# Kernel tuning notes

Hardware: AMD Instinct MI355X
Metric: run time of the kernel (lower is better)

Reference implementation:

```python
import jax, jax.numpy as jnp
import numpy as np

EPS = 1e-5

def conv1x1(x, w, b):
    # x: [B,C,H,W], w: [O,C], b: [O]
    return jnp.einsum('bchw,oc->bohw', x, w) + b[None, :, None, None]

def bn_eval(x, g, b, m, v):
    scale = g / jnp.sqrt(v + EPS)
    return x * scale[None, :, None, None] + (b - m * scale)[None, :, None, None]

def setup_inputs() -> dict:
    key = jax.random.key(0)
    ks = jax.random.split(key, 32)
    B, Ch, Cl, H, W = 8, 256, 128, 64, 64
    r = Cl // 2
    red = 16  # CBAM channel-attention reduction
    s = 0.05
    n = lambda k, shape: jax.random.normal(k, shape, dtype=jnp.float32) * s
    inp = {
        'x': jax.random.normal(ks[0], (B, Ch, H, W), dtype=jnp.float32),
        'x0': jax.random.normal(ks[1], (B, Cl, H, W), dtype=jnp.float32),
        # CNL (flag=0)
        'cnl_g_w': n(ks[2], (Cl, Cl)), 'cnl_g_b': n(ks[3], (Cl,)),
        'cnl_theta_w': n(ks[4], (Cl, Ch)), 'cnl_theta_b': n(ks[5], (Cl,)),
        'cnl_phi_w': n(ks[6], (Cl, Cl)), 'cnl_phi_b': n(ks[7], (Cl,)),
        'cnl_W_w': n(ks[8], (Ch, Cl)), 'cnl_W_b': n(ks[9], (Ch,)),
        'cnl_bn_g': n(ks[10], (Ch,)), 'cnl_bn_b': n(ks[11], (Ch,)),
        'cnl_bn_m': n(ks[12], (Ch,)),
        'cnl_bn_v': jax.random.uniform(ks[13], (Ch,), dtype=jnp.float32) + 0.5,
        # PNL (reduc_ratio=2)
        'pnl_g_w': n(ks[14], (r, Cl)), 'pnl_g_b': n(ks[15], (r,)),
        'pnl_theta_w': n(ks[16], (r, Ch)), 'pnl_theta_b': n(ks[17], (r,)),
        'pnl_phi_w': n(ks[18], (r, Cl)), 'pnl_phi_b': n(ks[19], (r,)),
        'pnl_W_w': n(ks[20], (Ch, r)), 'pnl_W_b': n(ks[21], (Ch,)),
        'pnl_bn_g': n(ks[22], (Ch,)), 'pnl_bn_b': n(ks[23], (Ch,)),
        'pnl_bn_m': n(ks[24], (Ch,)),
        'pnl_bn_v': jax.random.uniform(ks[25], (Ch,), dtype=jnp.float32) + 0.5,
        # CBAM
        'ca_fc1_w': n(ks[26], (Ch // red, Ch)),
        'ca_fc2_w': n(ks[27], (Ch, Ch // red)),
        'sa_conv_w': n(ks[28], (1, 2, 7, 7)),
        'fusion_weight': jnp.float32(0.5),
    }
    return inp

def mdfo_forward(x, x0, cnl_g_w, cnl_g_b, cnl_theta_w, cnl_theta_b, cnl_phi_w, cnl_phi_b,
                 cnl_W_w, cnl_W_b, cnl_bn_g, cnl_bn_b, cnl_bn_m, cnl_bn_v,
                 pnl_g_w, pnl_g_b, pnl_theta_w, pnl_theta_b, pnl_phi_w, pnl_phi_b,
                 pnl_W_w, pnl_W_b, pnl_bn_g, pnl_bn_b, pnl_bn_m, pnl_bn_v,
                 ca_fc1_w, ca_fc2_w, sa_conv_w, fusion_weight):
    B, Ch, H, W = x.shape
    Cl = x0.shape[1]
    N = H * W
    # ---- CNL (flag=0): channel-space affinity [B, Cl, Cl] ----
    g_x = conv1x1(x0, cnl_g_w, cnl_g_b).reshape(B, Cl, N)
    th = conv1x1(x, cnl_theta_w, cnl_theta_b).reshape(B, Cl, N)
    ph = conv1x1(x0, cnl_phi_w, cnl_phi_b).reshape(B, Cl, N)
    att = jnp.einsum('bcn,bdn->bcd', th, ph) / Cl  # energy / energy.size(-1)
    y = jnp.einsum('bcd,bdn->bcn', att, g_x).reshape(B, Cl, H, W)
    z_cnl = bn_eval(conv1x1(y, cnl_W_w, cnl_W_b), cnl_bn_g, cnl_bn_b, cnl_bn_m, cnl_bn_v) + x
    # ---- PNL: pixel-space affinity [B, N/2, N/2] (faithful channel-folding reshape) ----
    r = Cl // 2
    M = N // 2
    g2 = conv1x1(x0, pnl_g_w, pnl_g_b).reshape(B, Cl, M).transpose(0, 2, 1)          # [B,M,Cl]
    t2 = conv1x1(z_cnl, pnl_theta_w, pnl_theta_b).reshape(B, Cl, M).transpose(0, 2, 1)
    p2 = conv1x1(x0, pnl_phi_w, pnl_phi_b).reshape(B, Cl, M)
    att2 = jnp.einsum('bnc,bcm->bnm', t2, p2) / M
    y2 = jnp.einsum('bnm,bmc->bnc', att2, g2).transpose(0, 2, 1).reshape(B, r, H, W)
    z_pnl = bn_eval(conv1x1(y2, pnl_W_w, pnl_W_b), pnl_bn_g, pnl_bn_b, pnl_bn_m, pnl_bn_v) + z_cnl
    # ---- CBAM: channel attention then spatial attention ----
    def mlp(v):
        return jnp.einsum('bh,oh->bo', jax.nn.relu(jnp.einsum('bc,hc->bh', v, ca_fc1_w)), ca_fc2_w)
    ca = jax.nn.sigmoid(mlp(z_pnl.mean(axis=(2, 3))) + mlp(z_pnl.max(axis=(2, 3))))
    xc = z_pnl * ca[:, :, None, None]
    sa_in = jnp.concatenate([xc.mean(axis=1, keepdims=True), xc.max(axis=1, keepdims=True)], axis=1)
    sa = jax.lax.conv_general_dilated(sa_in, sa_conv_w, (1, 1), ((3, 3), (3, 3)),
                                      dimension_numbers=('NCHW', 'OIHW', 'NCHW'))
    z_cbam = xc * jax.nn.sigmoid(sa)
    # ---- weighted fusion (dropout is identity in eval mode) ----
    return fusion_weight * z_cbam + (1.0 - fusion_weight) * x

def reference(x, x0, cnl_g_w, cnl_g_b, cnl_theta_w, cnl_theta_b, cnl_phi_w, cnl_phi_b,
              cnl_W_w, cnl_W_b, cnl_bn_g, cnl_bn_b, cnl_bn_m, cnl_bn_v,
              pnl_g_w, pnl_g_b, pnl_theta_w, pnl_theta_b, pnl_phi_w, pnl_phi_b,
              pnl_W_w, pnl_W_b, pnl_bn_g, pnl_bn_b, pnl_bn_m, pnl_bn_v,
              ca_fc1_w, ca_fc2_w, sa_conv_w, fusion_weight):
    return mdfo_forward(x, x0, cnl_g_w, cnl_g_b, cnl_theta_w, cnl_theta_b, cnl_phi_w, cnl_phi_b,
                        cnl_W_w, cnl_W_b, cnl_bn_g, cnl_bn_b, cnl_bn_m, cnl_bn_v,
                        pnl_g_w, pnl_g_b, pnl_theta_w, pnl_theta_b, pnl_phi_w, pnl_phi_b,
                        pnl_W_w, pnl_W_b, pnl_bn_g, pnl_bn_b, pnl_bn_m, pnl_bn_v,
                        ca_fc1_w, ca_fc2_w, sa_conv_w, fusion_weight)
```

## Files before the change

### kernel.cpp

```cpp
#include <hip/hip_runtime.h>
#include <math.h>

typedef unsigned short u16;
typedef unsigned int   u32;
typedef __bf16 bf16_8 __attribute__((ext_vector_type(8)));
typedef float  f32x4  __attribute__((ext_vector_type(4)));

constexpr int BATCH = 8;
constexpr int CH    = 256;
constexpr int CL    = 128;
constexpr int NPIX  = 4096;
constexpr int HID   = 16;

__device__ __forceinline__ u16 f2bf(float f) {
    u32 u = __float_as_uint(f);
    u = (u + 0x7FFFu + ((u >> 16) & 1u)) >> 16;
    return (u16)u;
}
__device__ __forceinline__ float bf2f(u16 h) { return __uint_as_float((u32)h << 16); }
__device__ __forceinline__ u32 encF(float f) {
    u32 u = __float_as_uint(f);
    return u ^ (u32)(((int)u >> 31) | 0x80000000);
}
__device__ __forceinline__ float decF(u32 u) {
    return __uint_as_float((u >> 31) ? (u ^ 0x80000000u) : ~u);
}

template<int BN>
__global__ __launch_bounds__(256, 2)
void mfma_nt(const u16* __restrict__ A, long long sA, int lda,
             const u16* __restrict__ B, long long sB, int ldb,
             int K, int nSplit, int mode,
             u16* __restrict__ outB, float* __restrict__ outF, u32* __restrict__ maxOut,
             long long sC, int ldc,
             const float* __restrict__ bias, int biasRow,
             const float* __restrict__ bng, const float* __restrict__ bnb,
             const float* __restrict__ bnm, const float* __restrict__ bnv,
             const u16* __restrict__ resB, long long sR)
{
    constexpr int BM = 64, BK = 64;
    constexpr int WN = BN / 4;
    constexpr int NT = WN / 16;
    constexpr int SMSZ = BM * BK + BN * BK;
    __shared__ __align__(16) u16 smem[SMSZ + 0];
    u16* As = smem;
    u16* Bs = smem + BM * BK;
    u16* Ct = smem;
    float* sSum = (float*)&smem[BM * BN];
    u32*   sMax = (u32*)&smem[BM * BN + 512];

    const int bz    = blockIdx.z;
    const int batch = bz / nSplit;
    const int split = bz % nSplit;
    const int kLen  = K / nSplit;
    const int kBeg  = split * kLen;

    const u16* Ab = A + (size_t)batch * sA;
    const u16* Bb = B + (size_t)batch * sB;

    const int mBase = blockIdx.y * BM;
    const int nBase = blockIdx.x * BN;
    const int tid   = threadIdx.x;
    const int wave  = tid >> 6;
    const int lane  = tid & 63;
    const int lm    = lane & 15;
    const int q     = lane >> 4;

    f32x4 acc[4][NT];
#pragma unroll
    for (int i = 0; i < 4; ++i)
#pragma unroll
        for (int j = 0; j < NT; ++j) acc[i][j] = f32x4{0.f, 0.f, 0.f, 0.f};

    const int srow = tid >> 3;
    const int sc8  = tid & 7;

    for (int k0 = kBeg; k0 < kBeg + kLen; k0 += BK) {
        __syncthreads();
#pragma unroll
        for (int it = 0; it < 2; ++it) {
            int r = srow + it * 32;
            uint4 v = *(const uint4*)(Ab + (size_t)(mBase + r) * lda + k0 + sc8 * 8);
            *(uint4*)&As[r * BK + ((sc8 ^ (r & 7)) * 8)] = v;
        }
#pragma unroll
        for (int it = 0; it < BN / 32; ++it) {
            int r = srow + it * 32;
            uint4 v = *(const uint4*)(Bb + (size_t)(nBase + r) * ldb + k0 + sc8 * 8);
            *(uint4*)&Bs[r * BK + ((sc8 ^ (r & 7)) * 8)] = v;
        }
        __syncthreads();
#pragma unroll
        for (int ks = 0; ks < 2; ++ks) {
            bf16_8 af[4], bfr[NT];
#pragma unroll
            for (int mt = 0; mt < 4; ++mt) {
                int r = mt * 16 + lm;
                af[mt] = *(const bf16_8*)&As[r * BK + (((ks * 4 + q) ^ (lm & 7)) * 8)];
            }
#pragma unroll
            for (int nt = 0; nt < NT; ++nt) {
                int r = wave * WN + nt * 16 + lm;
                bfr[nt] = *(const bf16_8*)&Bs[r * BK + (((ks * 4 + q) ^ (lm & 7)) * 8)];
            }
#pragma unroll
            for (int mt = 0; mt < 4; ++mt)
#pragma unroll
                for (int nt = 0; nt < NT; ++nt)
                    acc[mt][nt] = __builtin_amdgcn_mfma_f32_16x16x32_bf16(
                        af[mt], bfr[nt], acc[mt][nt], 0, 0, 0);
        }
    }

    if (mode == 1) {
#pragma unroll
        for (int nt = 0; nt < NT; ++nt) {
            int col = nBase + wave * WN + nt * 16 + lm;
#pragma unroll
            for (int mt = 0; mt < 4; ++mt)
#pragma unroll
                for (int r = 0; r < 4; ++r) {
                    int row = mBase + mt * 16 + q * 4 + r;
                    atomicAdd(&outF[(size_t)batch * sC + (size_t)row * ldc + col],
                              acc[mt][nt][r]);
                }
        }
        return;
    }

    __syncthreads();
#pragma unroll
    for (int nt = 0; nt < NT; ++nt) {
        int lc = wave * WN + nt * 16 + lm;
#pragma unroll
        for (int mt = 0; mt < 4; ++mt)
#pragma unroll
            for (int r = 0; r < 4; ++r)
                Ct[(mt * 16 + q * 4 + r) * BN + lc] = f2bf(acc[mt][nt][r]);
    }
    __syncthreads();

    constexpr int CPR   = BN / 8;
    constexpr int RSTEP = 256 / CPR;
    constexpr int PT    = BM / RSTEP;
    const int cc  = (tid % CPR) * 8;
    const int lr0 = tid / CPR;

    float csc[8], csh[8], cbv[8];
    if (mode == 4 || mode == 5) {
#pragma unroll
        for (int j = 0; j < 8; ++j) {
            int C = nBase + cc + j;
            float sc = bng[C] * rsqrtf(bnv[C] + 1e-5f);
            csc[j] = sc;
            csh[j] = bnb[C] - bnm[C] * sc;
            cbv[j] = bias[C];
        }
    } else if ((mode == 0 || mode == 2) && bias && !biasRow) {
#pragma unroll
        for (int j = 0; j < 8; ++j) cbv[j] = bias[nBase + cc + j];
    } else {
#pragma unroll
        for (int j = 0; j < 8; ++j) cbv[j] = 0.f;
    }

    float tsum[8], tmax[8];
#pragma unroll
    for (int j = 0; j < 8; ++j) { tsum[j] = 0.f; tmax[j] = -1e30f; }

#pragma unroll
    for (int i = 0; i < PT; ++i) {
        int lr = lr0 + i * RSTEP;
        int R  = mBase + lr;
        uint4 raw = *(const uint4*)&Ct[lr * BN + cc];
        u32 w[4] = {raw.x, raw.y, raw.z, raw.w};
        float v[8];
#pragma unroll
        for (int jj = 0; jj < 4; ++jj) {
            v[2 * jj]     = bf2f((u16)(w[jj] & 0xFFFFu));
            v[2 * jj + 1] = bf2f((u16)(w[jj] >> 16));
        }
        if (mode == 0) {
            float rb = (bias && biasRow) ? bias[R] : 0.f;
            u32 o[4];
#pragma unroll
            for (int jj = 0; jj < 4; ++jj) {
                u16 lo = f2bf(v[2 * jj] + cbv[2 * jj] + rb);
                u16 hi = f2bf(v[2 * jj + 1] + cbv[2 * jj + 1] + rb);
                o[jj] = (u32)lo | ((u32)hi << 16);
            }
            *(uint4*)&outB[(size_t)batch * sC + (size_t)R * ldc + nBase + cc] =
                make_uint4(o[0], o[1], o[2], o[3]);
        } else if (mode == 2) {
            u32 o[4];
#pragma unroll
            for (int jj = 0; jj < 4; ++jj) {
                u16 lo = f2bf(v[2 * jj] + cbv[2 * jj]);
                u16 hi = f2bf(v[2 * jj + 1] + cbv[2 * jj + 1]);
                o[jj] = (u32)lo | ((u32)hi << 16);
            }
            size_t off = (size_t)batch * sC + (size_t)(R & 2047) * 128 + (R >> 11) * 64 + cc;
            *(uint4*)&outB[off] = make_uint4(o[0], o[1], o[2], o[3]);
        } else if (mode == 3) {
            u16 ev[4], od[4];
#pragma unroll
            for (int jj = 0; jj < 4; ++jj) {
                ev[jj] = f2bf(v[2 * jj]);
                od[jj] = f2bf(v[2 * jj + 1]);
            }
            int c0 = (cc >> 1);
            u32 e0 = (u32)ev[0] | ((u32)ev[1] << 16), e1 = (u32)ev[2] | ((u32)ev[3] << 16);
            u32 d0 = (u32)od[0] | ((u32)od[1] << 16), d1 = (u32)od[2] | ((u32)od[3] << 16);
            *(uint2*)&outB[(size_t)batch * sC + (size_t)R * 64 + c0] = make_uint2(e0, e1);
            *(uint2*)&outB[(size_t)batch * sC + (size_t)(R + 2048) * 64 + c0] = make_uint2(d0, d1);
        } else {
            size_t off = (size_t)batch * sC + (size_t)R * ldc + nBase + cc;
            uint4 rr = *(const uint4*)&resB[(size_t)batch * sR + (size_t)R * ldc + nBase + cc];
            u32 rw[4] = {rr.x, rr.y, rr.z, rr.w};
            u32 o[4];
#pragma unroll
            for (int jj = 0; jj < 4; ++jj) {
                float z0 = (v[2 * jj] + cbv[2 * jj]) * csc[2 * jj] + csh[2 * jj] +
                           bf2f((u16)(rw[jj] & 0xFFFFu));
                float z1 = (v[2 * jj + 1] + cbv[2 * jj + 1]) * csc[2 * jj + 1] + csh[2 * jj + 1] +
                           bf2f((u16)(rw[jj] >> 16));
                u16 lo = f2bf(z0), hi = f2bf(z1);
                o[jj] = (u32)lo | ((u32)hi << 16);
                tsum[2 * jj] += bf2f(lo);  tsum[2 * jj + 1] += bf2f(hi);
                tmax[2 * jj]   = fmaxf(tmax[2 * jj], bf2f(lo));
                tmax[2 * jj + 1] = fmaxf(tmax[2 * jj + 1], bf2f(hi));
            }
            *(uint4*)&outB[off] = make_uint4(o[0], o[1], o[2], o[3]);
        }
    }

    if (mode == 5) {
        sSum[tid] = 0.f; sMax[tid] = 0u;
        __syncthreads();
#pragma unroll
        for (int j = 0; j < 8; ++j) {
            atomicAdd(&sSum[cc + j], tsum[j]);
            atomicMax(&sMax[cc + j], encF(tmax[j]));
        }
        __syncthreads();
        atomicAdd(&outF[batch * CH + tid], sSum[tid]);
        atomicMax(&maxOut[batch * CH + tid], sMax[tid]);
    }
}

__global__ __launch_bounds__(256)
void tcast2(const float* __restrict__ x, u16* __restrict__ xTb,
            const float* __restrict__ x0, u16* __restrict__ x0Tb)
{
    __shared__ u16 T[64][68];
    const int b = blockIdx.z;
    const bool isX = blockIdx.y < 4;
    const int C = isX ? 256 : 128;
    const float* in = isX ? x : x0;
    u16* out = isX ? xTb : x0Tb;
    const int cb = (isX ? blockIdx.y : blockIdx.y - 4) * 64;
    const int nb = blockIdx.x * 64;
    const int tid = threadIdx.x;
    {
        int nl = tid & 63, cq = tid >> 6;
#pragma unroll
        for (int i = 0; i < 16; ++i) {
            int c = cq * 16 + i;
            T[c][nl] = f2bf(in[(size_t)b * C * NPIX + (size_t)(cb + c) * NPIX + nb + nl]);
        }
    }
    __syncthreads();
    {
        int cl = tid & 63, nq = tid >> 6;
#pragma unroll
        for (int i = 0; i < 16; ++i) {
            int n = nq * 16 + i;
            out[(size_t)b * NPIX * C + (size_t)(nb + n) * C + cb + cl] = T[cl][n];
        }
    }
}

__global__ __launch_bounds__(256)
void prep(const float* w0, const float* w1, const float* w2, const float* w3,
          const float* w4, const float* w5, const float* w6, const float* w7,
          const float* pgb, const float* ppb,
          float* __restrict__ zr, u16* __restrict__ wsb, float* __restrict__ pb128)
{
    int i = blockIdx.x * 256 + threadIdx.x;
    if (i < 266240) zr[i] = 0.f;
    int j = i - 266240;
    if (j >= 0 && j < 147456) {
        float v;
        if      (j < 32768)  v = w0[j];
        else if (j < 49152)  v = w1[j - 32768];
        else if (j < 65536)  v = w2[j - 49152];
        else if (j < 98304)  v = w3[j - 65536];
        else if (j < 106496) v = w4[j - 98304];
        else if (j < 114688) v = w5[j - 106496];
        else if (j < 131072) v = w6[j - 114688];
        else                 v = w7[j - 131072];
        wsb[j] = f2bf(v);
    }
    int k = i - 413696;
    if (k >= 0 && k < 128) pb128[k] = (k < 64) ? pgb[k] : ppb[k - 64];
}

__global__ void cast_scale(const float* __restrict__ in, u16* __restrict__ out,
                           float alpha, int n, int perm)
{
    int i = blockIdx.x * 256 + threadIdx.x;
    if (i >= n) return;
    int src = i;
    if (perm) {
        int d = i & 127;
        src = (i & ~127) + 2 * (d & 63) + (d >> 6);
    }
    out[i] = f2bf(in[src] * alpha);
}

__global__ __launch_bounds__(256)
void ca_mlp(const float* __restrict__ meanS, const u32* __restrict__ maxU,
            const float* __restrict__ fc1, const float* __restrict__ fc2,
            float* __restrict__ ca)
{
    const int b = blockIdx.x, tid = threadIdx.x;
    __shared__ float s_avg[CH], s_mx[CH], s_h[HID];
    s_avg[tid] = meanS[b * CH + tid] * (1.f / NPIX);
    s_mx[tid]  = decF(maxU[b * CH + tid]);
    __syncthreads();
    if (tid < HID) {
        float ha = 0.f, hm = 0.f;
        for (int c = 0; c < CH; ++c) {
            float w = fc1[tid * CH + c];
            ha += w * s_avg[c];
            hm += w * s_mx[c];
        }
        s_h[tid] = fmaxf(ha, 0.f) + fmaxf(hm, 0.f);
    }
    __syncthreads();
    float o = 0.f;
#pragma unroll
    for (int h = 0; h < HID; ++h) o += fc2[tid * HID + h] * s_h[h];
    ca[b * CH + tid] = 1.f / (1.f + expf(-o));
}

__global__ __launch_bounds__(256)
void sa_input(const u16* __restrict__ z, const float* __restrict__ ca,
              float* __restrict__ sain)
{
    __shared__ float s_ca[CH];
    const int b = blockIdx.y;
    const int tid = threadIdx.x;
    s_ca[tid] = ca[b * CH + tid];
    __syncthreads();
    const int p = tid >> 2, part = tid & 3;
    const int n = blockIdx.x * 64 + p;
    const uint4* zr = (const uint4*)(z + ((size_t)b * NPIX + n) * CH + part * 64);
    float s = 0.f, m = -1e30f;
#pragma unroll
    for (int i = 0; i < 8; ++i) {
        uint4 v = zr[i];
        u32 w[4] = {v.x, v.y, v.z, v.w};
#pragma unroll
        for (int j = 0; j < 4; ++j) {
            int c = part * 64 + i * 8 + j * 2;
            float a = bf2f((u16)(w[j] & 0xFFFFu)) * s_ca[c];
            float d = bf2f((u16)(w[j] >> 16)) * s_ca[c + 1];
            s += a + d;
            m = fmaxf(m, fmaxf(a, d));
        }
    }
    s += __shfl_xor(s, 1); s += __shfl_xor(s, 2);
    m = fmaxf(m, __shfl_xor(m, 1)); m = fmaxf(m, __shfl_xor(m, 2));
    if (part == 0) {
        sain[(size_t)b * 2 * NPIX + n] = s * (1.f / CH);
        sain[(size_t)b * 2 * NPIX + NPIX + n] = m;
    }
}

__global__ __launch_bounds__(256)
void sa_conv7(const float* __restrict__ sain, const float* __restrict__ w,
              float* __restrict__ sig)
{
    __shared__ float ws[98];
    const int tid = threadIdx.x;
    if (tid < 98) ws[tid] = w[tid];
    __syncthreads();
    const int b = blockIdx.y;
    const int n = blockIdx.x * 256 + tid;
    const int h = n >> 6, x = n & 63;
    const float* p = sain + (size_t)b * 2 * NPIX;
    float s = 0.f;
#pragma unroll
    for (int ci = 0; ci < 2; ++ci)
#pragma unroll
        for (int ky = 0; ky < 7; ++ky) {
            int yy = h + ky - 3;
            if (yy < 0 || yy >= 64) continue;
#pragma unroll
            for (int kx = 0; kx < 7; ++kx) {
                int xx = x + kx - 3;
                if (xx < 0 || xx >= 64) continue;
                s += ws[ci * 49 + ky * 7 + kx] * p[ci * NPIX + yy * 64 + xx];
            }
        }
    sig[(size_t)b * NPIX + n] = 1.f / (1.f + expf(-s));
}

__global__ __launch_bounds__(256)
void fuse_out(const u16* __restrict__ z, const float* __restrict__ ca,
              const float* __restrict__ sig, const float* __restrict__ x,
              const float* __restrict__ fwp, float* __restrict__ out)
{
    __shared__ float T[64][65];
    const int b = blockIdx.z;
    const int cb = blockIdx.y * 64;
    const int nb = blockIdx.x * 64;
    const int tid = threadIdx.x;
    const float fw = fwp[0];
    {
        int cl = tid & 63, nq = tid >> 6;
        float cav = ca[b * CH + cb + cl];
#pragma unroll
        for (int i = 0; i < 16; ++i) {
            int n = nq * 16 + i;
            float v = bf2f(z[(size_t)b * CH * NPIX + (size_t)(nb + n) * CH + cb + cl]);
            T[cl][n] = v * cav * sig[(size_t)b * NPIX + nb + n];
        }
    }
    __syncthreads();
    {
        int nl = tid & 63, cq = tid >> 6;
#pragma unroll
        for (int i = 0; i < 16; ++i) {
            int c = cq * 16 + i;
            size_t o = (size_t)b * CH * NPIX + (size_t)(cb + c) * NPIX + nb + nl;
            out[o] = fw * T[c][nl] + (1.f - fw) * x[o];
        }
    }
}

extern "C" void kernel_launch(void* const* d_in, const int* in_sizes, int n_in,
                              void* d_out, int out_size, void* d_ws, size_t ws_size,
                              hipStream_t stream)
{
    const float* x        = (const float*)d_in[0];
    const float* x0       = (const float*)d_in[1];
    const float* cnl_g_w  = (const float*)d_in[2];
    const float* cnl_g_b  = (const float*)d_in[3];
    const float* cnl_th_w = (const float*)d_in[4];
    const float* cnl_th_b = (const float*)d_in[5];
    const float* cnl_ph_w = (const float*)d_in[6];
    const float* cnl_ph_b = (const float*)d_in[7];
    const float* cnl_W_w  = (const float*)d_in[8];
    const float* cnl_W_b  = (const float*)d_in[9];
    const float* cnl_bn_g = (const float*)d_in[10];
    const float* cnl_bn_b = (const float*)d_in[11];
    const float* cnl_bn_m = (const float*)d_in[12];
    const float* cnl_bn_v = (const float*)d_in[13];
    const float* pnl_g_b  = (const float*)d_in[15];
    const float* pnl_th_b = (const float*)d_in[17];
    const float* pnl_ph_b = (const float*)d_in[19];
    const float* pnl_W_b  = (const float*)d_in[21];
    const float* pnl_bn_g = (const float*)d_in[22];
    const float* pnl_bn_b = (const float*)d_in[23];
    const float* pnl_bn_m = (const float*)d_in[24];
    const float* pnl_bn_v = (const float*)d_in[25];
    const float* ca_fc1   = (const float*)d_in[26];
    const float* ca_fc2   = (const float*)d_in[27];
    const float* sa_w     = (const float*)d_in[28];
    const float* fw       = (const float*)d_in[29];
    float* out = (float*)d_out;
    char* wsc  = (char*)d_ws;

    u16* xTb   = (u16*)(wsc + 0);
    u16* x0Tb  = (u16*)(wsc + 16777216);
    u16* g2p2  = (u16*)(wsc + 25165824);
    u16* thcn  = g2p2;
    u16* phcn  = (u16*)(wsc + 33554432);
    u16* gT    = (u16*)(wsc + 41943040);
    u16* yT    = (u16*)(wsc + 50331648);
    u16* zb    = (u16*)(wsc + 58720256);
    float* attF  = (float*)(wsc + 75497472);
    float* SF    = (float*)(wsc + 76021760);
    float* meanS = (float*)(wsc + 76546048);
    u32*   maxU  = (u32*)  (wsc + 76554240);
    u16* attb  = (u16*)(wsc + 76562432);
    u16* Sb    = (u16*)(wsc + 76824576);
    float* ca  = (float*)(wsc + 77086720);
    float* sain= (float*)(wsc + 77094912);
    float* sig = (float*)(wsc + 77357056);
    u16* wsb   = (u16*)(wsc + 77488128);
    float* pb128 = (float*)(wsc + 77783040);
    u16* T2f   = phcn;
    u16* Ync   = phcn + 2097152;

    u16* w_th = wsb + 0;
    u16* w_ph = wsb + 32768;
    u16* w_g  = wsb + 49152;
    u16* w_z  = wsb + 65536;
    u16* w_gp = wsb + 98304;
    u16* w_t2 = wsb + 114688;
    u16* w_zp = wsb + 131072;

    const dim3 blk(256);
    const long long sX  = (long long)NPIX * CH;
    const long long sX0 = (long long)NPIX * CL;
    const long long sCN = (long long)CL * NPIX;
    const long long sR2 = (long long)64 * NPIX;
    const long long sAt = (long long)CL * CL;

    prep<<<dim3(1617), blk, 0, stream>>>(cnl_th_w, cnl_ph_w, cnl_g_w, cnl_W_w,
        (const float*)d_in[14], (const float*)d_in[18], (const float*)d_in[16],
        (const float*)d_in[20], pnl_g_b, pnl_ph_b, attF, wsb, pb128);
    tcast2<<<dim3(64, 6, 8), blk, 0, stream>>>(x, xTb, x0, x0Tb);

    mfma_nt<256><<<dim3(16, 2, 8), blk, 0, stream>>>(w_th, 0, 256, xTb, sX, 256,
        256, 1, 0, thcn, nullptr, nullptr, sCN, 4096, cnl_th_b, 1,
        nullptr, nullptr, nullptr, nullptr, nullptr, 0);
    mfma_nt<256><<<dim3(16, 2, 8), blk, 0, stream>>>(w_ph, 0, 128, x0Tb, sX0, 128,
        128, 1, 0, phcn, nullptr, nullptr, sCN, 4096, cnl_ph_b, 1,
        nullptr, nullptr, nullptr, nullptr, nullptr, 0);
    mfma_nt<128><<<dim3(1, 64, 8), blk, 0, stream>>>(x0Tb, sX0, 128, w_g, 0, 128,
        128, 1, 0, gT, nullptr, nullptr, sX0, 128, cnl_g_b, 0,
        nullptr, nullptr, nullptr, nullptr, nullptr, 0);
    mfma_nt<128><<<dim3(1, 2, 128), blk, 0, stream>>>(thcn, sCN, 4096, phcn, sCN, 4096,
        4096, 16, 1, nullptr, attF, nullptr, sAt, 128, nullptr, 0,
        nullptr, nullptr, nullptr, nullptr, nullptr, 0);
    cast_scale<<<dim3(512), blk, 0, stream>>>(attF, attb, 1.f / CL, 131072, 0);
    mfma_nt<128><<<dim3(1, 64, 8), blk, 0, stream>>>(gT, sX0, 128, attb, sAt, 128,
        128, 1, 0, yT, nullptr, nullptr, sX0, 128, nullptr, 0,
        nullptr, nullptr, nullptr, nullptr, nullptr, 0);
    mfma_nt<256><<<dim3(1, 64, 8), blk, 0, stream>>>(yT, sX0, 128, w_z, 0, 128,
        128, 1, 4, zb, nullptr, nullptr, sX, 256, cnl_W_b, 0,
        cnl_bn_g, cnl_bn_b, cnl_bn_m, cnl_bn_v, xTb, sX);

    mfma_nt<256><<<dim3(16, 2, 8), blk, 0, stream>>>(w_gp, 0, 128, x0Tb, sX0, 128,
        128, 1, 0, g2p2, nullptr, nullptr, sCN, 4096, pb128, 1,
        nullptr, nullptr, nullptr, nullptr, nullptr, 0);
    mfma_nt<64><<<dim3(1, 64, 8), blk, 0, stream>>>(zb, sX, 256, w_t2, 0, 256,
        256, 1, 2, T2f, nullptr, nullptr, sR2, 128, pnl_th_b, 0,
        nullptr, nullptr, nullptr, nullptr, nullptr, 0);
    mfma_nt<128><<<dim3(1, 2, 64), blk, 0, stream>>>(g2p2, sCN, 2048, g2p2 + 262144, sCN, 2048,
        2048, 8, 1, nullptr, SF, nullptr, sAt, 128, nullptr, 0,
        nullptr, nullptr, nullptr, nullptr, nullptr, 0);
    cast_scale<<<dim3(512), blk, 0, stream>>>(SF, Sb, 1.f / 2048.f, 131072, 1);
    mfma_nt<128><<<dim3(1, 32, 8), blk, 0, stream>>>(T2f, sR2, 128, Sb, sAt, 128,
        128, 1, 3, Ync, nullptr, nullptr, sR2, 64, nullptr, 0,
        nullptr, nullptr, nullptr, nullptr, nullptr, 0);
    mfma_nt<256><<<dim3(1, 64, 8), blk, 0, stream>>>(Ync, sR2, 64, w_zp, 0, 64,
        64, 1, 5, zb, meanS, maxU, sX, 256, pnl_W_b, 0,
        pnl_bn_g, pnl_bn_b, pnl_bn_m, pnl_bn_v, zb, sX);

    ca_mlp<<<dim3(8), blk, 0, stream>>>(meanS, maxU, ca_fc1, ca_fc2, ca);
    sa_input<<<dim3(64, 8), blk, 0, stream>>>(zb, ca, sain);
    sa_conv7<<<dim3(16, 8), blk, 0, stream>>>(sain, sa_w, sig);
    fuse_out<<<dim3(64, 4, 8), blk, 0, stream>>>(zb, ca, sig, x, fw, out);
}
```

Baseline: 301.0 us.

## Batch independent GEMMs into grouped launches and fuse CNL output with PNL theta projection

New measurement: 261.7 us. 13.0% less time.

```diff
diff --git a/kernel.cpp b/kernel.cpp
--- a/kernel.cpp
+++ b/kernel.cpp
@@ -6,11 +6,8 @@
 typedef __bf16 bf16_8 __attribute__((ext_vector_type(8)));
 typedef float  f32x4  __attribute__((ext_vector_type(4)));
 
-constexpr int BATCH = 8;
-constexpr int CH    = 256;
-constexpr int CL    = 128;
-constexpr int NPIX  = 4096;
-constexpr int HID   = 16;
+constexpr int CH   = 256;
+constexpr int NPIX = 4096;
 
 __device__ __forceinline__ u16 f2bf(float f) {
     u32 u = __float_as_uint(f);
@@ -26,45 +23,55 @@
     return __uint_as_float((u >> 31) ? (u ^ 0x80000000u) : ~u);
 }
 
+struct GJob {
+    const u16* A; const u16* B;
+    u16* outB; float* outF; u32* maxOut;
+    const float* bias; const float* bng; const float* bnb; const float* bnm;
+    const float* bnv; const u16* resB;
+    long long sA, sB, sC, sR;
+    int lda, ldb, ldc, K, nSplit, mode, biasRow, gx, gy, nBlk;
+};
+struct GJobs { GJob j[4]; int n; };
+
 template<int BN>
 __global__ __launch_bounds__(256, 2)
-void mfma_nt(const u16* __restrict__ A, long long sA, int lda,
-             const u16* __restrict__ B, long long sB, int ldb,
-             int K, int nSplit, int mode,
-             u16* __restrict__ outB, float* __restrict__ outF, u32* __restrict__ maxOut,
-             long long sC, int ldc,
-             const float* __restrict__ bias, int biasRow,
-             const float* __restrict__ bng, const float* __restrict__ bnb,
-             const float* __restrict__ bnm, const float* __restrict__ bnv,
-             const u16* __restrict__ resB, long long sR)
+void mfma_multi(GJobs jobs)
 {
     constexpr int BM = 64, BK = 64;
     constexpr int WN = BN / 4;
     constexpr int NT = WN / 16;
-    constexpr int SMSZ = BM * BK + BN * BK;
-    __shared__ __align__(16) u16 smem[SMSZ + 0];
+    __shared__ __align__(16) u16 smem[BM * BK + BN * BK];
     u16* As = smem;
     u16* Bs = smem + BM * BK;
     u16* Ct = smem;
     float* sSum = (float*)&smem[BM * BN];
     u32*   sMax = (u32*)&smem[BM * BN + 512];
 
-    const int bz    = blockIdx.z;
-    const int batch = bz / nSplit;
-    const int split = bz % nSplit;
-    const int kLen  = K / nSplit;
-    const int kBeg  = split * kLen;
-
-    const u16* Ab = A + (size_t)batch * sA;
-    const u16* Bb = B + (size_t)batch * sB;
-
-    const int mBase = blockIdx.y * BM;
-    const int nBase = blockIdx.x * BN;
-    const int tid   = threadIdx.x;
-    const int wave  = tid >> 6;
-    const int lane  = tid & 63;
-    const int lm    = lane & 15;
-    const int q     = lane >> 4;
+    int ji = 0, start = 0;
+    {
+        int bxx = blockIdx.x;
+        while (ji + 1 < jobs.n && bxx >= start + jobs.j[ji].nBlk) {
+            start += jobs.j[ji].nBlk; ++ji;
+        }
+    }
+    const GJob J = jobs.j[ji];
+    const int local = blockIdx.x - start;
+    const int per = J.gx * J.gy;
+    const int bz = local / per;
+    const int r2 = local - bz * per;
+    const int by = r2 / J.gx;
+    const int bx2 = r2 - by * J.gx;
+    const int batch = bz / J.nSplit;
+    const int split = bz - batch * J.nSplit;
+    const int kLen = J.K / J.nSplit;
+    const int kBeg = split * kLen;
+
+    const u16* Ab = J.A + (size_t)batch * J.sA;
+    const u16* Bb = J.B + (size_t)batch * J.sB;
+    const int mBase = by * BM;
+    const int nBase = bx2 * BN;
+    const int tid = threadIdx.x;
+    const int wave = tid >> 6, lane = tid & 63, lm = lane & 15, q = lane >> 4;
 
     f32x4 acc[4][NT];
 #pragma unroll
@@ -72,21 +79,20 @@
 #pragma unroll
         for (int j = 0; j < NT; ++j) acc[i][j] = f32x4{0.f, 0.f, 0.f, 0.f};
 
-    const int srow = tid >> 3;
-    const int sc8  = tid & 7;
+    const int srow = tid >> 3, sc8 = tid & 7;
 
     for (int k0 = kBeg; k0 < kBeg + kLen; k0 += BK) {
         __syncthreads();
 #pragma unroll
         for (int it = 0; it < 2; ++it) {
             int r = srow + it * 32;
-            uint4 v = *(const uint4*)(Ab + (size_t)(mBase + r) * lda + k0 + sc8 * 8);
+            uint4 v = *(const uint4*)(Ab + (size_t)(mBase + r) * J.lda + k0 + sc8 * 8);
             *(uint4*)&As[r * BK + ((sc8 ^ (r & 7)) * 8)] = v;
         }
 #pragma unroll
         for (int it = 0; it < BN / 32; ++it) {
             int r = srow + it * 32;
-            uint4 v = *(const uint4*)(Bb + (size_t)(nBase + r) * ldb + k0 + sc8 * 8);
+            uint4 v = *(const uint4*)(Bb + (size_t)(nBase + r) * J.ldb + k0 + sc8 * 8);
             *(uint4*)&Bs[r * BK + ((sc8 ^ (r & 7)) * 8)] = v;
         }
         __syncthreads();
@@ -112,7 +118,7 @@
         }
     }
 
-    if (mode == 1) {
+    if (J.mode == 1) {
 #pragma unroll
         for (int nt = 0; nt < NT; ++nt) {
             int col = nBase + wave * WN + nt * 16 + lm;
@@ -121,7 +127,7 @@
 #pragma unroll
                 for (int r = 0; r < 4; ++r) {
                     int row = mBase + mt * 16 + q * 4 + r;
-                    atomicAdd(&outF[(size_t)batch * sC + (size_t)row * ldc + col],
+                    atomicAdd(&J.outF[(size_t)batch * J.sC + (size_t)row * J.ldc + col],
                               acc[mt][nt][r]);
                 }
         }
@@ -140,25 +146,25 @@
     }
     __syncthreads();
 
-    constexpr int CPR   = BN / 8;
+    constexpr int CPR = BN / 8;
     constexpr int RSTEP = 256 / CPR;
-    constexpr int PT    = BM / RSTEP;
-    const int cc  = (tid % CPR) * 8;
+    constexpr int PT = BM / RSTEP;
+    const int cc = (tid % CPR) * 8;
     const int lr0 = tid / CPR;
 
     float csc[8], csh[8], cbv[8];
-    if (mode == 4 || mode == 5) {
+    if (J.mode == 4 || J.mode == 5) {
 #pragma unroll
         for (int j = 0; j < 8; ++j) {
             int C = nBase + cc + j;
-            float sc = bng[C] * rsqrtf(bnv[C] + 1e-5f);
+            float sc = J.bng[C] * rsqrtf(J.bnv[C] + 1e-5f);
             csc[j] = sc;
-            csh[j] = bnb[C] - bnm[C] * sc;
-            cbv[j] = bias[C];
-        }
-    } else if ((mode == 0 || mode == 2) && bias && !biasRow) {
-#pragma unroll
-        for (int j = 0; j < 8; ++j) cbv[j] = bias[nBase + cc + j];
+            csh[j] = J.bnb[C] - J.bnm[C] * sc;
+            cbv[j] = J.bias[C];
+        }
+    } else if (J.mode == 0 && J.bias && !J.biasRow) {
+#pragma unroll
+        for (int j = 0; j < 8; ++j) cbv[j] = J.bias[nBase + cc + j];
     } else {
 #pragma unroll
         for (int j = 0; j < 8; ++j) cbv[j] = 0.f;
@@ -171,7 +177,7 @@
 #pragma unroll
     for (int i = 0; i < PT; ++i) {
         int lr = lr0 + i * RSTEP;
-        int R  = mBase + lr;
+        int R = mBase + lr;
         uint4 raw = *(const uint4*)&Ct[lr * BN + cc];
         u32 w[4] = {raw.x, raw.y, raw.z, raw.w};
         float v[8];
@@ -180,8 +186,8 @@
             v[2 * jj]     = bf2f((u16)(w[jj] & 0xFFFFu));
             v[2 * jj + 1] = bf2f((u16)(w[jj] >> 16));
         }
-        if (mode == 0) {
-            float rb = (bias && biasRow) ? bias[R] : 0.f;
+        if (J.mode == 0) {
+            float rb = (J.bias && J.biasRow) ? J.bias[R] : 0.f;
             u32 o[4];
 #pragma unroll
             for (int jj = 0; jj < 4; ++jj) {
@@ -189,19 +195,9 @@
                 u16 hi = f2bf(v[2 * jj + 1] + cbv[2 * jj + 1] + rb);
                 o[jj] = (u32)lo | ((u32)hi << 16);
             }
-            *(uint4*)&outB[(size_t)batch * sC + (size_t)R * ldc + nBase + cc] =
+            *(uint4*)&J.outB[(size_t)batch * J.sC + (size_t)R * J.ldc + nBase + cc] =
                 make_uint4(o[0], o[1], o[2], o[3]);
-        } else if (mode == 2) {
-            u32 o[4];
-#pragma unroll
-            for (int jj = 0; jj < 4; ++jj) {
-                u16 lo = f2bf(v[2 * jj] + cbv[2 * jj]);
-                u16 hi = f2bf(v[2 * jj + 1] + cbv[2 * jj + 1]);
-                o[jj] = (u32)lo | ((u32)hi << 16);
-            }
-            size_t off = (size_t)batch * sC + (size_t)(R & 2047) * 128 + (R >> 11) * 64 + cc;
-            *(uint4*)&outB[off] = make_uint4(o[0], o[1], o[2], o[3]);
-        } else if (mode == 3) {
+        } else if (J.mode == 3) {
             u16 ev[4], od[4];
 #pragma unroll
             for (int jj = 0; jj < 4; ++jj) {
@@ -211,30 +207,30 @@
             int c0 = (cc >> 1);
             u32 e0 = (u32)ev[0] | ((u32)ev[1] << 16), e1 = (u32)ev[2] | ((u32)ev[3] << 16);
             u32 d0 = (u32)od[0] | ((u32)od[1] << 16), d1 = (u32)od[2] | ((u32)od[3] << 16);
-            *(uint2*)&outB[(size_t)batch * sC + (size_t)R * 64 + c0] = make_uint2(e0, e1);
-            *(uint2*)&outB[(size_t)batch * sC + (size_t)(R + 2048) * 64 + c0] = make_uint2(d0, d1);
+            *(uint2*)&J.outB[(size_t)batch * J.sC + (size_t)R * 64 + c0] = make_uint2(e0, e1);
+            *(uint2*)&J.outB[(size_t)batch * J.sC + (size_t)(R + 2048) * 64 + c0] = make_uint2(d0, d1);
         } else {
-            size_t off = (size_t)batch * sC + (size_t)R * ldc + nBase + cc;
-            uint4 rr = *(const uint4*)&resB[(size_t)batch * sR + (size_t)R * ldc + nBase + cc];
+            size_t off = (size_t)batch * J.sC + (size_t)R * J.ldc + nBase + cc;
+            uint4 rr = *(const uint4*)&J.resB[(size_t)batch * J.sR + (size_t)R * J.ldc + nBase + cc];
             u32 rw[4] = {rr.x, rr.y, rr.z, rr.w};
             u32 o[4];
 #pragma unroll
             for (int jj = 0; jj < 4; ++jj) {
                 float z0 = (v[2 * jj] + cbv[2 * jj]) * csc[2 * jj] + csh[2 * jj] +
                            bf2f((u16)(rw[jj] & 0xFFFFu));
-                float z1 = (v[2 * jj + 1] + cbv[2 * jj + 1]) * csc[2 * jj + 1] + csh[2 * jj + 1] +
-                           bf2f((u16)(rw[jj] >> 16));
+                float z1 = (v[2 * jj + 1] + cbv[2 * jj + 1]) * csc[2 * jj + 1] +
+                           csh[2 * jj + 1] + bf2f((u16)(rw[jj] >> 16));
                 u16 lo = f2bf(z0), hi = f2bf(z1);
                 o[jj] = (u32)lo | ((u32)hi << 16);
-                tsum[2 * jj] += bf2f(lo);  tsum[2 * jj + 1] += bf2f(hi);
-                tmax[2 * jj]   = fmaxf(tmax[2 * jj], bf2f(lo));
+                tsum[2 * jj] += bf2f(lo); tsum[2 * jj + 1] += bf2f(hi);
+                tmax[2 * jj] = fmaxf(tmax[2 * jj], bf2f(lo));
                 tmax[2 * jj + 1] = fmaxf(tmax[2 * jj + 1], bf2f(hi));
             }
-            *(uint4*)&outB[off] = make_uint4(o[0], o[1], o[2], o[3]);
-        }
-    }
-
-    if (mode == 5) {
+            *(uint4*)&J.outB[off] = make_uint4(o[0], o[1], o[2], o[3]);
+        }
+    }
+
+    if (J.mode == 5) {
         sSum[tid] = 0.f; sMax[tid] = 0u;
         __syncthreads();
 #pragma unroll
@@ -243,92 +239,236 @@
             atomicMax(&sMax[cc + j], encF(tmax[j]));
         }
         __syncthreads();
-        atomicAdd(&outF[batch * CH + tid], sSum[tid]);
-        atomicMax(&maxOut[batch * CH + tid], sMax[tid]);
-    }
+        atomicAdd(&J.outF[batch * CH + tid], sSum[tid]);
+        atomicMax(&J.maxOut[batch * CH + tid], sMax[tid]);
+    }
+}
+
+__global__ __launch_bounds__(256, 2)
+void zcnl_t2(const u16* __restrict__ yTg, const u16* __restrict__ w_z,
+             const u16* __restrict__ xTb, const u16* __restrict__ w_t2,
+             u16* __restrict__ zb, u16* __restrict__ T2f,
+             const float* __restrict__ bias,
+             const float* __restrict__ bng, const float* __restrict__ bnb,
+             const float* __restrict__ bnm, const float* __restrict__ bnv,
+             const float* __restrict__ bias2)
+{
+    constexpr int BM = 64, BK = 64, BN = 256, WN = 64, NT = 4;
+    constexpr int LDP = 264;
+    __shared__ __align__(16) u16 smem[33792];
+    u16* As = smem;
+    u16* Bs = smem + 4096;
+    u16* Ct = smem;
+    u16* B2 = smem + 16896;
+
+    const int batch = blockIdx.z;
+    const int mBase = blockIdx.y * BM;
+    const int tid = threadIdx.x;
+    const int wave = tid >> 6, lane = tid & 63, lm = lane & 15, q = lane >> 4;
+    const u16* Ab = yTg + (size_t)batch * 524288;
+
+    f32x4 acc[4][NT];
+#pragma unroll
+    for (int i = 0; i < 4; ++i)
+#pragma unroll
+        for (int j = 0; j < NT; ++j) acc[i][j] = f32x4{0.f, 0.f, 0.f, 0.f};
+
+    const int srow = tid >> 3, sc8 = tid & 7;
+    for (int k0 = 0; k0 < 128; k0 += BK) {
+        __syncthreads();
+#pragma unroll
+        for (int it = 0; it < 2; ++it) {
+            int r = srow + it * 32;
+            uint4 v = *(const uint4*)(Ab + (size_t)(mBase + r) * 128 + k0 + sc8 * 8);
+            *(uint4*)&As[r * BK + ((sc8 ^ (r & 7)) * 8)] = v;
+        }
+#pragma unroll
+        for (int it = 0; it < 8; ++it) {
+            int r = srow + it * 32;
+            uint4 v = *(const uint4*)(w_z + (size_t)r * 128 + k0 + sc8 * 8);
+            *(uint4*)&Bs[r * BK + ((sc8 ^ (r & 7)) * 8)] = v;
+        }
+        __syncthreads();
+#pragma unroll
+        for (int ks = 0; ks < 2; ++ks) {
+            bf16_8 af[4], bfr[NT];
+#pragma unroll
+            for (int mt = 0; mt < 4; ++mt) {
+                int r = mt * 16 + lm;
+                af[mt] = *(const bf16_8*)&As[r * BK + (((ks * 4 + q) ^ (lm & 7)) * 8)];
+            }
+#pragma unroll
+            for (int nt = 0; nt < NT; ++nt) {
+                int r = wave * WN + nt * 16 + lm;
+                bfr[nt] = *(const bf16_8*)&Bs[r * BK + (((ks * 4 + q) ^ (lm & 7)) * 8)];
+            }
+#pragma unroll
+            for (int mt = 0; mt < 4; ++mt)
+#pragma unroll
+                for (int nt = 0; nt < NT; ++nt)
+                    acc[mt][nt] = __builtin_amdgcn_mfma_f32_16x16x32_bf16(
+                        af[mt], bfr[nt], acc[mt][nt], 0, 0, 0);
+        }
+    }
+
+    __syncthreads();
+#pragma unroll
+    for (int nt = 0; nt < NT; ++nt) {
+        int lc = wave * WN + nt * 16 + lm;
+#pragma unroll
+        for (int mt = 0; mt < 4; ++mt)
+#pragma unroll
+            for (int r = 0; r < 4; ++r)
+                Ct[(mt * 16 + q * 4 + r) * LDP + lc] = f2bf(acc[mt][nt][r]);
+    }
+#pragma unroll
+    for (int i = 0; i < 8; ++i) {
+        int id = tid + i * 256;
+        int r = id >> 5, ch = id & 31;
+        *(uint4*)&B2[r * LDP + ch * 8] = *(const uint4*)(w_t2 + r * 256 + ch * 8);
+    }
+    __syncthreads();
+
+    const int cc = (tid & 31) * 8;
+    const int lr0 = tid >> 5;
+    float csc[8], csh[8], cbv[8];
+#pragma unroll
+    for (int j = 0; j < 8; ++j) {
+        int C = cc + j;
+        float sc = bng[C] * rsqrtf(bnv[C] + 1e-5f);
+        csc[j] = sc;
+        csh[j] = bnb[C] - bnm[C] * sc;
+        cbv[j] = bias[C];
+    }
+#pragma unroll
+    for (int i = 0; i < 8; ++i) {
+        int lr = lr0 + i * 8;
+        int R = mBase + lr;
+        uint4 raw = *(const uint4*)&Ct[lr * LDP + cc];
+        u32 w[4] = {raw.x, raw.y, raw.z, raw.w};
+        uint4 rr = *(const uint4*)&xTb[(size_t)batch * 1048576 + (size_t)R * 256 + cc];
+        u32 rw[4] = {rr.x, rr.y, rr.z, rr.w};
+        u32 o[4];
+#pragma unroll
+        for (int jj = 0; jj < 4; ++jj) {
+            float z0 = (bf2f((u16)(w[jj] & 0xFFFFu)) + cbv[2 * jj]) * csc[2 * jj] +
+                       csh[2 * jj] + bf2f((u16)(rw[jj] & 0xFFFFu));
+            float z1 = (bf2f((u16)(w[jj] >> 16)) + cbv[2 * jj + 1]) * csc[2 * jj + 1] +
+                       csh[2 * jj + 1] + bf2f((u16)(rw[jj] >> 16));
+            o[jj] = (u32)f2bf(z0) | ((u32)f2bf(z1) << 16);
+        }
+        *(uint4*)&zb[(size_t)batch * 1048576 + (size_t)R * 256 + cc] =
+            make_uint4(o[0], o[1], o[2], o[3]);
+        *(uint4*)&Ct[lr * LDP + cc] = make_uint4(o[0], o[1], o[2], o[3]);
+    }
+    __syncthreads();
+
+    f32x4 acc2[4];
+#pragma unroll
+    for (int i = 0; i < 4; ++i) acc2[i] = f32x4{0.f, 0.f, 0.f, 0.f};
+#pragma unroll
+    for (int ks = 0; ks < 8; ++ks) {
+        bf16_8 bf = *(const bf16_8*)&B2[(wave * 16 + lm) * LDP + ks * 32 + q * 8];
+#pragma unroll
+        for (int mt = 0; mt < 4; ++mt) {
+            bf16_8 af = *(const bf16_8*)&Ct[(mt * 16 + lm) * LDP + ks * 32 + q * 8];
+            acc2[mt] = __builtin_amdgcn_mfma_f32_16x16x32_bf16(af, bf, acc2[mt], 0, 0, 0);
+        }
+    }
+    const int d = wave * 16 + lm;
+    const float b2v = bias2[d];
+#pragma unroll
+    for (int mt = 0; mt < 4; ++mt)
+#pragma unroll
+        for (int r = 0; r < 4; ++r) {
+            int pix = mBase + mt * 16 + q * 4 + r;
+            T2f[(size_t)batch * 262144 + (size_t)(pix & 2047) * 128 + (pix >> 11) * 64 + d] =
+                f2bf(acc2[mt][r] + b2v);
+        }
 }
 
 __global__ __launch_bounds__(256)
-void tcast2(const float* __restrict__ x, u16* __restrict__ xTb,
-            const float* __restrict__ x0, u16* __restrict__ x0Tb)
+void prep_tcast(const float* __restrict__ x, u16* __restrict__ xTb,
+                const float* __restrict__ x0, u16* __restrict__ x0Tb,
+                const float* w0, const float* w1, const float* w2, const float* w3,
+                const float* w4, const float* w5, const float* w6, const float* w7,
+                const float* pgb, const float* ppb,
+                float* __restrict__ zr, u16* __restrict__ wsb, float* __restrict__ pb128)
 {
     __shared__ u16 T[64][68];
-    const int b = blockIdx.z;
-    const bool isX = blockIdx.y < 4;
-    const int C = isX ? 256 : 128;
-    const float* in = isX ? x : x0;
-    u16* out = isX ? xTb : x0Tb;
-    const int cb = (isX ? blockIdx.y : blockIdx.y - 4) * 64;
-    const int nb = blockIdx.x * 64;
-    const int tid = threadIdx.x;
-    {
-        int nl = tid & 63, cq = tid >> 6;
-#pragma unroll
-        for (int i = 0; i < 16; ++i) {
-            int c = cq * 16 + i;
-            T[c][nl] = f2bf(in[(size_t)b * C * NPIX + (size_t)(cb + c) * NPIX + nb + nl]);
-        }
-    }
-    __syncthreads();
-    {
-        int cl = tid & 63, nq = tid >> 6;
-#pragma unroll
-        for (int i = 0; i < 16; ++i) {
-            int n = nq * 16 + i;
-            out[(size_t)b * NPIX * C + (size_t)(nb + n) * C + cb + cl] = T[cl][n];
-        }
+    const int bx = blockIdx.x, tid = threadIdx.x;
+    if (bx < 3072) {
+        const int b = bx / 384, rem = bx % 384;
+        const int by = rem / 64, nb = (rem % 64) * 64;
+        const bool isX = by < 4;
+        const int C = isX ? 256 : 128;
+        const float* in = isX ? x : x0;
+        u16* out = isX ? xTb : x0Tb;
+        const int cb = (isX ? by : by - 4) * 64;
+        {
+            int nl = tid & 63, cq = tid >> 6;
+#pragma unroll
+            for (int i = 0; i < 16; ++i) {
+                int c = cq * 16 + i;
+                T[c][nl] = f2bf(in[(size_t)b * C * NPIX + (size_t)(cb + c) * NPIX + nb + nl]);
+            }
+        }
+        __syncthreads();
+        {
+            int cl = tid & 63, nq = tid >> 6;
+#pragma unroll
+            for (int i = 0; i < 16; ++i) {
+                int n = nq * 16 + i;
+                out[(size_t)b * NPIX * C + (size_t)(nb + n) * C + cb + cl] = T[cl][n];
+            }
+        }
+    } else {
+        int i = (bx - 3072) * 256 + tid;
+        if (i < 266240) zr[i] = 0.f;
+        int j = i - 266240;
+        if (j >= 0 && j < 147456) {
+            float v;
+            if      (j < 32768)  v = w0[j];
+            else if (j < 49152)  v = w1[j - 32768];
+            else if (j < 65536)  v = w2[j - 49152];
+            else if (j < 98304)  v = w3[j - 65536];
+            else if (j < 106496) v = w4[j - 98304];
+            else if (j < 114688) v = w5[j - 106496];
+            else if (j < 131072) v = w6[j - 114688];
+            else                 v = w7[j - 131072];
+            wsb[j] = f2bf(v);
+        }
+        int k = i - 413696;
+        if (k >= 0 && k < 128) pb128[k] = (k < 64) ? pgb[k] : ppb[k - 64];
+    }
+}
+
+__global__ void cast2(const float* __restrict__ attF, u16* __restrict__ attb,
+                      const float* __restrict__ SF, u16* __restrict__ Sb)
+{
+    int i = blockIdx.x * 256 + threadIdx.x;
+    if (i < 131072) {
+        attb[i] = f2bf(attF[i] * (1.f / 128.f));
+    } else {
+        int j = i - 131072;
+        int dd = j & 127;
+        int src = (j & ~127) + 2 * (dd & 63) + (dd >> 6);
+        Sb[j] = f2bf(SF[src] * (1.f / 2048.f));
     }
 }
 
 __global__ __launch_bounds__(256)
-void prep(const float* w0, const float* w1, const float* w2, const float* w3,
-          const float* w4, const float* w5, const float* w6, const float* w7,
-          const float* pgb, const float* ppb,
-          float* __restrict__ zr, u16* __restrict__ wsb, float* __restrict__ pb128)
-{
-    int i = blockIdx.x * 256 + threadIdx.x;
-    if (i < 266240) zr[i] = 0.f;
-    int j = i - 266240;
-    if (j >= 0 && j < 147456) {
-        float v;
-        if      (j < 32768)  v = w0[j];
-        else if (j < 49152)  v = w1[j - 32768];
-        else if (j < 65536)  v = w2[j - 49152];
-        else if (j < 98304)  v = w3[j - 65536];
-        else if (j < 106496) v = w4[j - 98304];
-        else if (j < 114688) v = w5[j - 106496];
-        else if (j < 131072) v = w6[j - 114688];
-        else                 v = w7[j - 131072];
-        wsb[j] = f2bf(v);
-    }
-    int k = i - 413696;
-    if (k >= 0 && k < 128) pb128[k] = (k < 64) ? pgb[k] : ppb[k - 64];
-}
-
-__global__ void cast_scale(const float* __restrict__ in, u16* __restrict__ out,
-                           float alpha, int n, int perm)
-{
-    int i = blockIdx.x * 256 + threadIdx.x;
-    if (i >= n) return;
-    int src = i;
-    if (perm) {
-        int d = i & 127;
-        src = (i & ~127) + 2 * (d & 63) + (d >> 6);
-    }
-    out[i] = f2bf(in[src] * alpha);
-}
-
-__global__ __launch_bounds__(256)
-void ca_mlp(const float* __restrict__ meanS, const u32* __restrict__ maxU,
-            const float* __restrict__ fc1, const float* __restrict__ fc2,
-            float* __restrict__ ca)
-{
-    const int b = blockIdx.x, tid = threadIdx.x;
-    __shared__ float s_avg[CH], s_mx[CH], s_h[HID];
+void sa_ca(const u16* __restrict__ z, const float* __restrict__ meanS,
+           const u32* __restrict__ maxU, const float* __restrict__ fc1,
+           const float* __restrict__ fc2, float* __restrict__ ca,
+           float* __restrict__ sain)
+{
+    const int b = blockIdx.y, tid = threadIdx.x;
+    __shared__ float s_avg[CH], s_mx[CH], s_h[16], s_ca[CH];
     s_avg[tid] = meanS[b * CH + tid] * (1.f / NPIX);
     s_mx[tid]  = decF(maxU[b * CH + tid]);
     __syncthreads();
-    if (tid < HID) {
+    if (tid < 16) {
         float ha = 0.f, hm = 0.f;
         for (int c = 0; c < CH; ++c) {
             float w = fc1[tid * CH + c];
@@ -340,19 +480,12 @@
     __syncthreads();
     float o = 0.f;
 #pragma unroll
-    for (int h = 0; h < HID; ++h) o += fc2[tid * HID + h] * s_h[h];
-    ca[b * CH + tid] = 1.f / (1.f + expf(-o));
-}
-
-__global__ __launch_bounds__(256)
-void sa_input(const u16* __restrict__ z, const float* __restrict__ ca,
-              float* __restrict__ sain)
-{
-    __shared__ float s_ca[CH];
-    const int b = blockIdx.y;
-    const int tid = threadIdx.x;
-    s_ca[tid] = ca[b * CH + tid];
-    __syncthreads();
+    for (int h = 0; h < 16; ++h) o += fc2[tid * 16 + h] * s_h[h];
+    float cav = 1.f / (1.f + expf(-o));
+    s_ca[tid] = cav;
+    if (blockIdx.x == 0) ca[b * CH + tid] = cav;
+    __syncthreads();
+
     const int p = tid >> 2, part = tid & 3;
     const int n = blockIdx.x * 64 + p;
     const uint4* zr = (const uint4*)(z + ((size_t)b * NPIX + n) * CH + part * 64);
@@ -379,44 +512,37 @@
 }
 
 __global__ __launch_bounds__(256)
-void sa_conv7(const float* __restrict__ sain, const float* __restrict__ w,
-              float* __restrict__ sig)
+void fuse_conv(const u16* __restrict__ z, const float* __restrict__ ca,
+               const float* __restrict__ sain, const float* __restrict__ sa_w,
+               const float* __restrict__ x, const float* __restrict__ fwp,
+               float* __restrict__ out)
 {
     __shared__ float ws[98];
+    __shared__ float s_sig[64];
+    __shared__ float T[64][65];
+    const int b = blockIdx.z, cb = blockIdx.y * 64, h = blockIdx.x;
+    const int nb = h * 64;
     const int tid = threadIdx.x;
-    if (tid < 98) ws[tid] = w[tid];
-    __syncthreads();
-    const int b = blockIdx.y;
-    const int n = blockIdx.x * 256 + tid;
-    const int h = n >> 6, x = n & 63;
-    const float* p = sain + (size_t)b * 2 * NPIX;
-    float s = 0.f;
-#pragma unroll
-    for (int ci = 0; ci < 2; ++ci)
+    if (tid < 98) ws[tid] = sa_w[tid];
+    __syncthreads();
+    if (tid < 64) {
+        const float* p = sain + (size_t)b * 2 * NPIX;
+        float s = 0.f;
 #pragma unroll
         for (int ky = 0; ky < 7; ++ky) {
             int yy = h + ky - 3;
             if (yy < 0 || yy >= 64) continue;
 #pragma unroll
             for (int kx = 0; kx < 7; ++kx) {
-                int xx = x + kx - 3;
+                int xx = tid + kx - 3;
                 if (xx < 0 || xx >= 64) continue;
-                s += ws[ci * 49 + ky * 7 + kx] * p[ci * NPIX + yy * 64 + xx];
-            }
-        }
-    sig[(size_t)b * NPIX + n] = 1.f / (1.f + expf(-s));
-}
-
-__global__ __launch_bounds__(256)
-void fuse_out(const u16* __restrict__ z, const float* __restrict__ ca,
-              const float* __restrict__ sig, const float* __restrict__ x,
-              const float* __restrict__ fwp, float* __restrict__ out)
-{
-    __shared__ float T[64][65];
-    const int b = blockIdx.z;
-    const int cb = blockIdx.y * 64;
-    const int nb = blockIdx.x * 64;
-    const int tid = threadIdx.x;
+                s += ws[ky * 7 + kx] * p[yy * 64 + xx] +
+                     ws[49 + ky * 7 + kx] * p[NPIX + yy * 64 + xx];
+            }
+        }
+        s_sig[tid] = 1.f / (1.f + expf(-s));
+    }
+    __syncthreads();
     const float fw = fwp[0];
     {
         int cl = tid & 63, nq = tid >> 6;
@@ -424,8 +550,8 @@
 #pragma unroll
         for (int i = 0; i < 16; ++i) {
             int n = nq * 16 + i;
-            float v = bf2f(z[(size_t)b * CH * NPIX + (size_t)(nb + n) * CH + cb + cl]);
-            T[cl][n] = v * cav * sig[(size_t)b * NPIX + nb + n];
+            float v = bf2f(z[((size_t)b * NPIX + nb + n) * CH + cb + cl]);
+            T[cl][n] = v * cav * s_sig[n];
         }
     }
     __syncthreads();
@@ -438,6 +564,23 @@
             out[o] = fw * T[c][nl] + (1.f - fw) * x[o];
         }
     }
+}
+
+static GJob mkjob(const u16* A, const u16* B, u16* outB, float* outF, u32* maxOut,
+                  const float* bias, const float* bng, const float* bnb,
+                  const float* bnm, const float* bnv, const u16* resB,
+                  long long sA, long long sB, long long sC, long long sR,
+                  int lda, int ldb, int ldc, int K, int nSplit, int mode,
+                  int biasRow, int gx, int gy)
+{
+    GJob g;
+    g.A = A; g.B = B; g.outB = outB; g.outF = outF; g.maxOut = maxOut;
+    g.bias = bias; g.bng = bng; g.bnb = bnb; g.bnm = bnm; g.bnv = bnv; g.resB = resB;
+    g.sA = sA; g.sB = sB; g.sC = sC; g.sR = sR;
+    g.lda = lda; g.ldb = ldb; g.ldc = ldc; g.K = K; g.nSplit = nSplit;
+    g.mode = mode; g.biasRow = biasRow; g.gx = gx; g.gy = gy;
+    g.nBlk = gx * gy * 8 * nSplit;
+    return g;
 }
 
 extern "C" void kernel_launch(void* const* d_in, const int* in_sizes, int n_in,
@@ -458,9 +601,13 @@
     const float* cnl_bn_b = (const float*)d_in[11];
     const float* cnl_bn_m = (const float*)d_in[12];
     const float* cnl_bn_v = (const float*)d_in[13];
+    const float* pnl_g_w  = (const float*)d_in[14];
     const float* pnl_g_b  = (const float*)d_in[15];
+    const float* pnl_th_w = (const float*)d_in[16];
     const float* pnl_th_b = (const float*)d_in[17];
+    const float* pnl_ph_w = (const float*)d_in[18];
     const float* pnl_ph_b = (const float*)d_in[19];
+    const float* pnl_W_w  = (const float*)d_in[20];
     const float* pnl_W_b  = (const float*)d_in[21];
     const float* pnl_bn_g = (const float*)d_in[22];
     const float* pnl_bn_b = (const float*)d_in[23];
@@ -475,23 +622,22 @@
 
     u16* xTb   = (u16*)(wsc + 0);
     u16* x0Tb  = (u16*)(wsc + 16777216);
-    u16* g2p2  = (u16*)(wsc + 25165824);
-    u16* thcn  = g2p2;
+    u16* thcn  = (u16*)(wsc + 25165824);
     u16* phcn  = (u16*)(wsc + 33554432);
     u16* gT    = (u16*)(wsc + 41943040);
     u16* yT    = (u16*)(wsc + 50331648);
     u16* zb    = (u16*)(wsc + 58720256);
-    float* attF  = (float*)(wsc + 75497472);
-    float* SF    = (float*)(wsc + 76021760);
-    float* meanS = (float*)(wsc + 76546048);
-    u32*   maxU  = (u32*)  (wsc + 76554240);
-    u16* attb  = (u16*)(wsc + 76562432);
-    u16* Sb    = (u16*)(wsc + 76824576);
-    float* ca  = (float*)(wsc + 77086720);
-    float* sain= (float*)(wsc + 77094912);
-    float* sig = (float*)(wsc + 77357056);
-    u16* wsb   = (u16*)(wsc + 77488128);
-    float* pb128 = (float*)(wsc + 77783040);
+    u16* g2p2  = (u16*)(wsc + 75497472);
+    float* attF  = (float*)(wsc + 83886080);
+    float* SF    = (float*)(wsc + 84410368);
+    float* meanS = (float*)(wsc + 84934656);
+    u32*   maxU  = (u32*)  (wsc + 84942848);
+    u16* attb  = (u16*)(wsc + 84951040);
+    u16* Sb    = (u16*)(wsc + 85213184);
+    float* ca  = (float*)(wsc + 85475328);
+    float* sain= (float*)(wsc + 85483520);
+    u16* wsb   = (u16*)(wsc + 85745664);
+    float* pb128 = (float*)(wsc + 86040576);
     u16* T2f   = phcn;
     u16* Ync   = phcn + 2097152;
 
@@ -503,57 +649,51 @@
     u16* w_t2 = wsb + 114688;
     u16* w_zp = wsb + 131072;
 
-    const dim3 blk(256);
-    const long long sX  = (long long)NPIX * CH;
-    const long long sX0 = (long long)NPIX * CL;
-    const long long sCN = (long long)CL * NPIX;
-    const long long sR2 = (long long)64 * NPIX;
-    const long long sAt = (long long)CL * CL;
-
-    prep<<<dim3(1617), blk, 0, stream>>>(cnl_th_w, cnl_ph_w, cnl_g_w, cnl_W_w,
-        (const float*)d_in[14], (const float*)d_in[18], (const float*)d_in[16],
-        (const float*)d_in[20], pnl_g_b, pnl_ph_b, attF, wsb, pb128);
-    tcast2<<<dim3(64, 6, 8), blk, 0, stream>>>(x, xTb, x0, x0Tb);
-
-    mfma_nt<256><<<dim3(16, 2, 8), blk, 0, stream>>>(w_th, 0, 256, xTb, sX, 256,
-        256, 1, 0, thcn, nullptr, nullptr, sCN, 4096, cnl_th_b, 1,
-        nullptr, nullptr, nullptr, nullptr, nullptr, 0);
-    mfma_nt<256><<<dim3(16, 2, 8), blk, 0, stream>>>(w_ph, 0, 128, x0Tb, sX0, 128,
-        128, 1, 0, phcn, nullptr, nullptr, sCN, 4096, cnl_ph_b, 1,
-        nullptr, nullptr, nullptr, nullptr, nullptr, 0);
-    mfma_nt<128><<<dim3(1, 64, 8), blk, 0, stream>>>(x0Tb, sX0, 128, w_g, 0, 128,
-        128, 1, 0, gT, nullptr, nullptr, sX0, 128, cnl_g_b, 0,
-        nullptr, nullptr, nullptr, nullptr, nullptr, 0);
-    mfma_nt<128><<<dim3(1, 2, 128), blk, 0, stream>>>(thcn, sCN, 4096, phcn, sCN, 4096,
-        4096, 16, 1, nullptr, attF, nullptr, sAt, 128, nullptr, 0,
-        nullptr, nullptr, nullptr, nullptr, nullptr, 0);
-    cast_scale<<<dim3(512), blk, 0, stream>>>(attF, attb, 1.f / CL, 131072, 0);
-    mfma_nt<128><<<dim3(1, 64, 8), blk, 0, stream>>>(gT, sX0, 128, attb, sAt, 128,
-        128, 1, 0, yT, nullptr, nullptr, sX0, 128, nullptr, 0,
-        nullptr, nullptr, nullptr, nullptr, nullptr, 0);
-    mfma_nt<256><<<dim3(1, 64, 8), blk, 0, stream>>>(yT, sX0, 128, w_z, 0, 128,
-        128, 1, 4, zb, nullptr, nullptr, sX, 256, cnl_W_b, 0,
-        cnl_bn_g, cnl_bn_b, cnl_bn_m, cnl_bn_v, xTb, sX);
-
-    mfma_nt<256><<<dim3(16, 2, 8), blk, 0, stream>>>(w_gp, 0, 128, x0Tb, sX0, 128,
-        128, 1, 0, g2p2, nullptr, nullptr, sCN, 4096, pb128, 1,
-        nullptr, nullptr, nullptr, nullptr, nullptr, 0);
-    mfma_nt<64><<<dim3(1, 64, 8), blk, 0, stream>>>(zb, sX, 256, w_t2, 0, 256,
-        256, 1, 2, T2f, nullptr, nullptr, sR2, 128, pnl_th_b, 0,
-        nullptr, nullptr, nullptr, nullptr, nullptr, 0);
-    mfma_nt<128><<<dim3(1, 2, 64), blk, 0, stream>>>(g2p2, sCN, 2048, g2p2 + 262144, sCN, 2048,
-        2048, 8, 1, nullptr, SF, nullptr, sAt, 128, nullptr, 0,
-        nullptr, nullptr, nullptr, nullptr, nullptr, 0);
-    cast_scale<<<dim3(512), blk, 0, stream>>>(SF, Sb, 1.f / 2048.f, 131072, 1);
-    mfma_nt<128><<<dim3(1, 32, 8), blk, 0, stream>>>(T2f, sR2, 128, Sb, sAt, 128,
-        128, 1, 3, Ync, nullptr, nullptr, sR2, 64, nullptr, 0,
-        nullptr, nullptr, nullptr, nullptr, nullptr, 0);
-    mfma_nt<256><<<dim3(1, 64, 8), blk, 0, stream>>>(Ync, sR2, 64, w_zp, 0, 64,
-        64, 1, 5, zb, meanS, maxU, sX, 256, pnl_W_b, 0,
-        pnl_bn_g, pnl_bn_b, pnl_bn_m, pnl_bn_v, zb, sX);
-
-    ca_mlp<<<dim3(8), blk, 0, stream>>>(meanS, maxU, ca_fc1, ca_fc2, ca);
-    sa_input<<<dim3(64, 8), blk, 0, stream>>>(zb, ca, sain);
-    sa_conv7<<<dim3(16, 8), blk, 0, stream>>>(sain, sa_w, sig);
-    fuse_out<<<dim3(64, 4, 8), blk, 0, stream>>>(zb, ca, sig, x, fw, out);
-}
+    const long long sX  = 1048576, sX0 = 524288, sCN = 524288, sAt = 16384;
+
+    prep_tcast<<<dim3(4689), dim3(256), 0, stream>>>(x, xTb, x0, x0Tb,
+        cnl_th_w, cnl_ph_w, cnl_g_w, cnl_W_w, pnl_g_w, pnl_ph_w, pnl_th_w, pnl_W_w,
+        pnl_g_b, pnl_ph_b, attF, wsb, pb128);
+
+    GJobs L1{}; L1.n = 4;
+    L1.j[0] = mkjob(w_th, xTb, thcn, 0, 0, cnl_th_b, 0, 0, 0, 0, 0,
+                    0, sX, sCN, 0, 256, 256, 4096, 256, 1, 0, 1, 32, 2);
+    L1.j[1] = mkjob(w_ph, x0Tb, phcn, 0, 0, cnl_ph_b, 0, 0, 0, 0, 0,
+                    0, sX0, sCN, 0, 128, 128, 4096, 128, 1, 0, 1, 32, 2);
+    L1.j[2] = mkjob(x0Tb, w_g, gT, 0, 0, cnl_g_b, 0, 0, 0, 0, 0,
+                    sX0, 0, sX0, 0, 128, 128, 128, 128, 1, 0, 0, 1, 64);
+    L1.j[3] = mkjob(w_gp, x0Tb, g2p2, 0, 0, pb128, 0, 0, 0, 0, 0,
+                    0, sX0, sCN, 0, 128, 128, 4096, 128, 1, 0, 1, 32, 2);
+    mfma_multi<128><<<dim3(2048), dim3(256), 0, stream>>>(L1);
+
+    GJobs SK{}; SK.n = 2;
+    SK.j[0] = mkjob(thcn, phcn, 0, attF, 0, 0, 0, 0, 0, 0, 0,
+                    sCN, sCN, sAt, 0, 4096, 4096, 128, 4096, 16, 1, 0, 1, 2);
+    SK.j[1] = mkjob(g2p2, g2p2 + 262144, 0, SF, 0, 0, 0, 0, 0, 0, 0,
+                    sCN, sCN, sAt, 0, 2048, 2048, 128, 2048, 8, 1, 0, 1, 2);
+    mfma_multi<128><<<dim3(384), dim3(256), 0, stream>>>(SK);
+
+    cast2<<<dim3(1024), dim3(256), 0, stream>>>(attF, attb, SF, Sb);
+
+    GJobs JY{}; JY.n = 1;
+    JY.j[0] = mkjob(gT, attb, yT, 0, 0, 0, 0, 0, 0, 0, 0,
+                    sX0, sAt, sX0, 0, 128, 128, 128, 128, 1, 0, 0, 1, 64);
+    mfma_multi<128><<<dim3(512), dim3(256), 0, stream>>>(JY);
+
+    zcnl_t2<<<dim3(1, 64, 8), dim3(256), 0, stream>>>(yT, w_z, xTb, w_t2, zb, T2f,
+        cnl_W_b, cnl_bn_g, cnl_bn_b, cnl_bn_m, cnl_bn_v, pnl_th_b);
+
+    GJobs JG{}; JG.n = 1;
+    JG.j[0] = mkjob(T2f, Sb, Ync, 0, 0, 0, 0, 0, 0, 0, 0,
+                    262144, sAt, 262144, 0, 128, 128, 64, 128, 1, 3, 0, 1, 32);
+    mfma_multi<128><<<dim3(256), dim3(256), 0, stream>>>(JG);
+
+    GJobs JZ{}; JZ.n = 1;
+    JZ.j[0] = mkjob(Ync, w_zp, zb, meanS, maxU, pnl_W_b,
+                    pnl_bn_g, pnl_bn_b, pnl_bn_m, pnl_bn_v, zb,
+                    262144, 0, sX, sX, 64, 64, 256, 64, 1, 5, 0, 1, 64);
+    mfma_multi<256><<<dim3(512), dim3(256), 0, stream>>>(JZ);
+
+    sa_ca<<<dim3(64, 8), dim3(256), 0, stream>>>(zb, meanS, maxU, ca_fc1, ca_fc2, ca, sain);
+    fuse_conv<<<dim3(64, 4, 8), dim3(256), 0, stream>>>(zb, ca, sain, sa_w, x, fw, out);
+}
```
